# Optimization experiments

Measured on AMD Instinct MI355X. Metric: run time of the kernel, lower is better.

The kernel has to match this reference:

```python
import jax, jax.numpy as jnp
import numpy as np


def setup_inputs() -> dict:
    key = jax.random.key(0)
    ks = jax.random.split(key, 5)
    t, b, s, d = 4, 4, 1024, 512
    x = jax.random.normal(ks[0], (t, b, s, d), dtype=jnp.float32)
    wq = jax.random.normal(ks[1], (d, d), dtype=jnp.float32) * 0.02
    wk = jax.random.normal(ks[2], (d, d), dtype=jnp.float32) * 0.02
    wv = jax.random.normal(ks[3], (d, d), dtype=jnp.float32) * 0.02
    wo = jax.random.normal(ks[4], (d, d), dtype=jnp.float32) * 0.02
    z = jnp.zeros((d,), dtype=jnp.float32)
    return {"x": x, "wq": wq, "bq": z, "wk": wk, "bk": z, "wv": wv,
            "bv": z, "wo": wo, "bo": z, "num_heads": 8}


def reference(x, wq, bq, wk, bk, wv, bv, wo, bo, num_heads):
    t, b, s, d = x.shape
    dh = d // num_heads
    # QKV projections (torch Linear stores weight as [out,in]; here weights are
    # random square matrices so x @ w + b is the same math)
    q = x @ wq + bq
    k = x @ wk + bk
    v = x @ wv + bv
    # Faithful to source: plain row-major view to (t*b*h, s, dh) WITHOUT
    # transposing a head axis (this mixes seq blocks into the batch-of-heads dim)
    q = q.reshape(t * b * num_heads, s, dh)
    k = k.reshape(t * b * num_heads, s, dh)
    v = v.reshape(t * b * num_heads, s, dh)
    scale = 1.0 / jnp.sqrt(jnp.float32(dh))
    scores = jnp.einsum('bqd,bkd->bqk', q, k) * scale  # [t*b*h, s, s]
    attn = jax.nn.softmax(scores, axis=-1)
    out = jnp.einsum('bqk,bkd->bqd', attn, v)  # [t*b*h, s, dh]
    out = out.reshape(t, b, s, d)
    return out @ wo + bo
```

## Files before the change

### kernel.cpp

```cpp
#include <hip/hip_runtime.h>

typedef __bf16 bf16;
typedef __bf16 bf16x4 __attribute__((ext_vector_type(4)));
typedef __bf16 bf16x8 __attribute__((ext_vector_type(8)));
typedef float  f32x4  __attribute__((ext_vector_type(4)));
typedef float  f32x16 __attribute__((ext_vector_type(16)));
typedef unsigned int u32x2 __attribute__((ext_vector_type(2)));
typedef unsigned int u32x4 __attribute__((ext_vector_type(4)));

#define MFMA16(a, b, c) __builtin_amdgcn_mfma_f32_16x16x32_bf16((a), (b), (c), 0, 0, 0)
#define MFMA32(a, b, c) __builtin_amdgcn_mfma_f32_32x32x16_bf16((a), (b), (c), 0, 0, 0)
#define SW(row, g) (((row) << 6) + ((((g) ^ ((row) & 7))) << 3))

#define QSCALE 0.1803368801111137f

typedef __attribute__((address_space(3))) uint32_t       lds_u32_t;
typedef const __attribute__((address_space(1))) uint32_t glob_u32_t;

__device__ __forceinline__ void ld_lds16(const bf16* g, bf16* l) {
    __builtin_amdgcn_global_load_lds((glob_u32_t*)g, (lds_u32_t*)l, 16, 0, 0);
}

template<int OFF>
__device__ __forceinline__ u32x2 tr_b16(uint32_t va) {
    u32x2 d;
    asm volatile("ds_read_b64_tr_b16 %0, %1 offset:%2"
                 : "=v"(d) : "v"(va), "n"(OFF));
    return d;
}

__global__ __launch_bounds__(256) void prep(
    const float* __restrict__ X,
    const float* __restrict__ wq, const float* __restrict__ wk,
    const float* __restrict__ wv, const float* __restrict__ wo,
    bf16* __restrict__ Xb, bf16* __restrict__ wqkvT, bf16* __restrict__ woT)
{
    int bid = blockIdx.x;
    if (bid < 4096) {
        size_t i = ((size_t)bid * 256 + threadIdx.x) * 8;
        const f32x4* s = (const f32x4*)(X + i);
        f32x4 a = s[0], b = s[1];
        bf16x8 o;
        for (int e = 0; e < 4; e++) { o[e] = (bf16)a[e]; o[e + 4] = (bf16)b[e]; }
        *(bf16x8*)(Xb + i) = o;
    } else {
        int idx = (bid - 4096) * 256 + threadIdx.x;
        int which = idx >> 15;
        int r = idx & 32767;
        int kg = r >> 9, n = r & 511;
        const float* w = (which == 0) ? wq : (which == 1) ? wk : (which == 2) ? wv : wo;
        bf16x8 o;
        for (int e = 0; e < 8; e++) o[e] = (bf16)w[(size_t)(kg * 8 + e) * 512 + n];
        bf16* dst = ((which < 3) ? (wqkvT + (size_t)which * 262144) : woT) + (size_t)n * 512 + kg * 8;
        *(bf16x8*)dst = o;
    }
}

__global__ __launch_bounds__(256, 4) void gemm_qkv(
    const bf16* __restrict__ Xb, const bf16* __restrict__ WT,
    const float* __restrict__ bq, const float* __restrict__ bk,
    const float* __restrict__ bv,
    bf16* __restrict__ Q, bf16* __restrict__ K, bf16* __restrict__ V)
{
    __shared__ char smem[34816];
    bf16* As = (bf16*)smem;
    bf16* Bs = (bf16*)(smem + 16384);

    const int t = threadIdx.x;
    const int lane = t & 63, wid = t >> 6;
    const int wr = wid >> 1, wc = wid & 1;
    const int lr = lane & 15, quad = lane >> 4;
    const int bid = blockIdx.x;
    const int xcd = bid & 7, j0 = bid >> 3;
    const int m0 = (xcd * 16 + (j0 & 15)) * 128;
    const int x = j0 >> 4;
    const int which = x >> 2;
    const int n0 = (x & 3) * 128;
    const bf16* Wt = WT + (size_t)which * 262144;

    f32x4 zf = {0.f, 0.f, 0.f, 0.f};
    f32x4 acc[4][4];
    for (int i = 0; i < 4; i++)
        for (int jj = 0; jj < 4; jj++) acc[i][jj] = zf;

    const int srow = t >> 3;
    const int sg = (t & 7) ^ (srow & 7);
    const bf16* gA = Xb + (size_t)(m0 + srow) * 512 + sg * 8;
    const bf16* gB = Wt + (size_t)(n0 + srow) * 512 + sg * 8;
    bf16* lA = As + t * 8;
    bf16* lB = Bs + t * 8;

    for (int k0 = 0; k0 < 512; k0 += 64) {
        for (int p = 0; p < 4; p++) {
            ld_lds16(gA + k0 + p * 32 * 512, lA + p * 2048);
            ld_lds16(gB + k0 + p * 32 * 512, lB + p * 2048);
        }
        __syncthreads();
        for (int kk = 0; kk < 2; ++kk) {
            bf16x8 af[4], bf_[4];
            for (int i = 0; i < 4; i++)
                af[i] = *(const bf16x8*)&As[SW(wr * 64 + i * 16 + lr, kk * 4 + quad)];
            for (int jj = 0; jj < 4; jj++)
                bf_[jj] = *(const bf16x8*)&Bs[SW(wc * 64 + jj * 16 + lr, kk * 4 + quad)];
            for (int i = 0; i < 4; i++)
                for (int jj = 0; jj < 4; jj++)
                    acc[i][jj] = MFMA16(af[i], bf_[jj], acc[i][jj]);
        }
        __syncthreads();
    }

    bf16* OUT = (which == 0) ? Q : (which == 1) ? K : V;
    const float* bias = (which == 0) ? bq : (which == 1) ? bk : bv;
    const float qs = (which == 0) ? QSCALE : 1.0f;

    bf16* Ep = (bf16*)smem + wid * 4352;
    for (int jj = 0; jj < 4; jj++) {
        int n = n0 + wc * 64 + jj * 16 + lr;
        float bb = bias[n];
        for (int i = 0; i < 4; i++) {
            int row = i * 16 + quad * 4;
            for (int r = 0; r < 4; r++)
                Ep[(row + r) * 68 + jj * 16 + lr] = (bf16)((acc[i][jj][r] + bb) * qs);
        }
    }
    bf16* wO = OUT + (size_t)(m0 + wr * 64) * 512 + n0 + wc * 64;
    for (int s = 0; s < 8; s++) {
        int row = s * 8 + (lane >> 3), g = lane & 7;
        *(bf16x8*)(wO + (size_t)row * 512 + g * 8) = *(const bf16x8*)&Ep[row * 68 + g * 8];
    }
}

__global__ __launch_bounds__(256, 4) void gemm_out(
    const bf16* __restrict__ A, const bf16* __restrict__ WoT,
    const float* __restrict__ bo, float* __restrict__ OUT)
{
    __shared__ char smem[34816];
    bf16* As = (bf16*)smem;
    bf16* Bs = (bf16*)(smem + 16384);

    const int t = threadIdx.x;
    const int lane = t & 63, wid = t >> 6;
    const int wr = wid >> 1, wc = wid & 1;
    const int lr = lane & 15, quad = lane >> 4;
    const int bid = blockIdx.x;
    const int xcd = bid & 7, j0 = bid >> 3;
    const int m0 = (xcd * 16 + (j0 & 15)) * 128;
    const int n0 = (j0 >> 4) * 128;

    f32x4 zf = {0.f, 0.f, 0.f, 0.f};
    f32x4 acc[4][4];
    for (int i = 0; i < 4; i++)
        for (int jj = 0; jj < 4; jj++) acc[i][jj] = zf;

    const int srow = t >> 3;
    const int sg = (t & 7) ^ (srow & 7);
    const bf16* gA = A + (size_t)(m0 + srow) * 512 + sg * 8;
    const bf16* gB = WoT + (size_t)(n0 + srow) * 512 + sg * 8;
    bf16* lA = As + t * 8;
    bf16* lB = Bs + t * 8;

    for (int k0 = 0; k0 < 512; k0 += 64) {
        for (int p = 0; p < 4; p++) {
            ld_lds16(gA + k0 + p * 32 * 512, lA + p * 2048);
            ld_lds16(gB + k0 + p * 32 * 512, lB + p * 2048);
        }
        __syncthreads();
        for (int kk = 0; kk < 2; ++kk) {
            bf16x8 af[4], bf_[4];
            for (int i = 0; i < 4; i++)
                af[i] = *(const bf16x8*)&As[SW(wr * 64 + i * 16 + lr, kk * 4 + quad)];
            for (int jj = 0; jj < 4; jj++)
                bf_[jj] = *(const bf16x8*)&Bs[SW(wc * 64 + jj * 16 + lr, kk * 4 + quad)];
            for (int i = 0; i < 4; i++)
                for (int jj = 0; jj < 4; jj++)
                    acc[i][jj] = MFMA16(af[i], bf_[jj], acc[i][jj]);
        }
        __syncthreads();
    }

    float bb[4];
    for (int jj = 0; jj < 4; jj++) bb[jj] = bo[n0 + wc * 64 + jj * 16 + lr];

    float* Ef = (float*)smem + wid * 2112;
    for (int h = 0; h < 2; h++) {
        for (int jj = 0; jj < 4; jj++)
            for (int ii = 0; ii < 2; ii++) {
                int i = h * 2 + ii;
                int row = ii * 16 + quad * 4;
                for (int r = 0; r < 4; r++)
                    Ef[(row + r) * 66 + jj * 16 + lr] = acc[i][jj][r] + bb[jj];
            }
        float* wO = OUT + (size_t)(m0 + wr * 64 + h * 32) * 512 + n0 + wc * 64;
        for (int s = 0; s < 8; s++) {
            int row = s * 4 + (lane >> 4), c = (lane & 15) * 4;
            *(f32x4*)(wO + (size_t)row * 512 + c) = *(const f32x4*)&Ef[row * 66 + c];
        }
        __syncthreads();
    }
}

__global__ __launch_bounds__(256, 4) void attn(
    const bf16* __restrict__ Q, const bf16* __restrict__ K,
    const bf16* __restrict__ V, bf16* __restrict__ O)
{
    __shared__ char smem[32768];
    bf16* const K0 = (bf16*)smem;
    bf16* const V0 = (bf16*)(smem + 8192);
    bf16* const K1 = (bf16*)(smem + 16384);
    bf16* const V1 = (bf16*)(smem + 24576);

    const int t = threadIdx.x, lane = t & 63, wid = t >> 6;
    const int q31 = lane & 31, hi = lane >> 5;
    const int bid = blockIdx.x;
    const int batch = (bid & 7) * 16 + ((bid >> 3) & 15);
    const int q0 = (bid >> 7) * 128;
    const bf16* Qb = Q + (size_t)batch * 65536;
    const bf16* Kb = K + (size_t)batch * 65536;
    const bf16* Vb = V + (size_t)batch * 65536;

    bf16x8 qf[4];
#pragma unroll
    for (int kk = 0; kk < 4; ++kk)
        qf[kk] = *(const bf16x8*)(Qb + (size_t)(q0 + wid * 32 + q31) * 64 + kk * 16 + hi * 8);

    f32x16 oacc[2];
#pragma unroll
    for (int ct = 0; ct < 2; ++ct)
#pragma unroll
        for (int r = 0; r < 16; ++r) oacc[ct][r] = 0.f;
    float lsum = 0.f;

    const int srow = t >> 3;
    const int sg8 = ((t & 7) ^ (srow & 7)) * 8;
    const int vkey = ((t >> 5) << 2) | ((t >> 1) & 3);
    const int vdh  = (((t >> 3) & 3) << 4) | ((t & 1) << 3);

#define STAGE(ktile, KD, VD) do {                                        \
        const bf16* gK_ = Kb + (size_t)(ktile) * 4096;                   \
        const bf16* gV_ = Vb + (size_t)(ktile) * 4096;                   \
        ld_lds16(gK_ + srow * 64 + sg8,          (KD) + t * 8);          \
        ld_lds16(gK_ + (srow + 32) * 64 + sg8,   (KD) + t * 8 + 2048);   \
        ld_lds16(gV_ + vkey * 64 + vdh,          (VD) + t * 8);          \
        ld_lds16(gV_ + (vkey + 32) * 64 + vdh,   (VD) + t * 8 + 2048);   \
    } while (0)

    const uint32_t vaL = ((uint32_t)hi << 10) + (((lane >> 4) & 1) << 7) + ((lane & 15) << 3);
    const uint32_t vaV0 = vaL + 8192u, vaV1 = vaL + 24576u;

    STAGE(0, K0, V0);

    for (int kt = 0; kt < 16; ++kt) {
        bf16* Kt = (kt & 1) ? K1 : K0;
        bf16* Kn = (kt & 1) ? K0 : K1;
        bf16* Vn = (kt & 1) ? V0 : V1;
        const uint32_t va = (kt & 1) ? vaV1 : vaV0;

        __builtin_amdgcn_sched_barrier(0);
        __builtin_amdgcn_s_barrier();
        __builtin_amdgcn_sched_barrier(0);
        if (kt < 15) {
            STAGE(kt + 1, Kn, Vn);
            asm volatile("s_waitcnt vmcnt(4)" ::: "memory");
        } else {
            asm volatile("s_waitcnt vmcnt(0)" ::: "memory");
        }
        __builtin_amdgcn_sched_barrier(0);
        __builtin_amdgcn_s_barrier();
        __builtin_amdgcn_sched_barrier(0);

        f32x16 sacc[2];
#pragma unroll
        for (int i2 = 0; i2 < 2; ++i2)
#pragma unroll
            for (int r = 0; r < 16; ++r) sacc[i2][r] = 0.f;

        __builtin_amdgcn_s_setprio(1);
#pragma unroll
        for (int kk = 0; kk < 4; ++kk) {
            bf16x8 a0 = *(const bf16x8*)&Kt[SW(q31, kk * 2 + hi)];
            bf16x8 a1 = *(const bf16x8*)&Kt[SW(32 + q31, kk * 2 + hi)];
            sacc[0] = MFMA32(a0, qf[kk], sacc[0]);
            sacc[1] = MFMA32(a1, qf[kk], sacc[1]);
        }
        __builtin_amdgcn_s_setprio(0);

        float ls = 0.f;
#pragma unroll
        for (int i2 = 0; i2 < 2; ++i2)
#pragma unroll
            for (int r = 0; r < 16; ++r) {
                float p = __builtin_amdgcn_exp2f(sacc[i2][r]);
                ls += p;
                sacc[i2][r] = p;
            }
        lsum += ls;

        bf16x8 pa[4];
#pragma unroll
        for (int c = 0; c < 4; ++c) {
            const int i2 = c >> 1, rb = (c & 1) * 8;
            uint32_t x0, x1, x2, x3;
            asm("v_cvt_pk_bf16_f32 %0, %1, %2" : "=v"(x0) : "v"(sacc[i2][rb + 0]), "v"(sacc[i2][rb + 1]));
            asm("v_cvt_pk_bf16_f32 %0, %1, %2" : "=v"(x1) : "v"(sacc[i2][rb + 2]), "v"(sacc[i2][rb + 3]));
            asm("v_cvt_pk_bf16_f32 %0, %1, %2" : "=v"(x2) : "v"(sacc[i2][rb + 4]), "v"(sacc[i2][rb + 5]));
            asm("v_cvt_pk_bf16_f32 %0, %1, %2" : "=v"(x3) : "v"(sacc[i2][rb + 6]), "v"(sacc[i2][rb + 7]));
            asm volatile("v_permlane32_swap_b32 %0, %1" : "+v"(x0), "+v"(x2));
            asm volatile("v_permlane32_swap_b32 %0, %1" : "+v"(x1), "+v"(x3));
            u32x4 w = {x0, x1, x2, x3};
            pa[c] = __builtin_bit_cast(bf16x8, w);
        }

        u32x2 tv[4][2][2];
#define TRPAIR(c, ct) do {                                               \
        tv[c][ct][0] = tr_b16<(c) * 2048 + (ct) * 256>(va);              \
        tv[c][ct][1] = tr_b16<(c) * 2048 + (ct) * 256 + 512>(va);        \
    } while (0)
        TRPAIR(0, 0); TRPAIR(0, 1);
        TRPAIR(1, 0); TRPAIR(1, 1);
        TRPAIR(2, 0); TRPAIR(2, 1);
        TRPAIR(3, 0); TRPAIR(3, 1);
#undef TRPAIR

        asm volatile("s_waitcnt lgkmcnt(0)" ::: "memory");
        __builtin_amdgcn_sched_barrier(0);
        __builtin_amdgcn_s_setprio(1);
#pragma unroll
        for (int c = 0; c < 4; ++c)
#pragma unroll
            for (int ct = 0; ct < 2; ++ct) {
                u32x4 w = {tv[c][ct][0][0], tv[c][ct][0][1],
                           tv[c][ct][1][0], tv[c][ct][1][1]};
                oacc[ct] = MFMA32(pa[c], __builtin_bit_cast(bf16x8, w), oacc[ct]);
            }
        __builtin_amdgcn_s_setprio(0);
    }
#undef STAGE

    lsum += __shfl_xor(lsum, 32, 64);
    const float invl = 1.f / lsum;

    __syncthreads();
    bf16* Ep = (bf16*)smem + wid * 2176;
#pragma unroll
    for (int r = 0; r < 16; ++r) {
        const int ql = (r & 3) + 8 * (r >> 2) + 4 * hi;
        const float im = __shfl(invl, ql, 64);
        Ep[ql * 68 + q31]      = (bf16)(oacc[0][r] * im);
        Ep[ql * 68 + 32 + q31] = (bf16)(oacc[1][r] * im);
    }
    bf16* Ob = O + (size_t)batch * 65536 + (size_t)(q0 + wid * 32) * 64;
#pragma unroll
    for (int s = 0; s < 4; s++) {
        int row = s * 8 + (lane >> 3), g = lane & 7;
        *(bf16x8*)(Ob + (size_t)row * 64 + g * 8) = *(const bf16x8*)&Ep[row * 68 + g * 8];
    }
}

extern "C" void kernel_launch(void* const* d_in, const int* in_sizes, int n_in,
                              void* d_out, int out_size, void* d_ws, size_t ws_size,
                              hipStream_t stream)
{
    const float* x  = (const float*)d_in[0];
    const float* wq = (const float*)d_in[1];
    const float* bq = (const float*)d_in[2];
    const float* wk = (const float*)d_in[3];
    const float* bk = (const float*)d_in[4];
    const float* wv = (const float*)d_in[5];
    const float* bv = (const float*)d_in[6];
    const float* wo = (const float*)d_in[7];
    const float* bo = (const float*)d_in[8];

    char* ws = (char*)d_ws;
    bf16* wqkvT = (bf16*)ws;
    bf16* woT   = (bf16*)(ws + 1572864);
    bf16* Xb    = (bf16*)(ws + 2097152);
    bf16* Qb    = (bf16*)(ws + 2097152 + 16777216ull);
    bf16* Kb    = (bf16*)(ws + 2097152 + 2 * 16777216ull);
    bf16* Vb    = (bf16*)(ws + 2097152 + 3 * 16777216ull);
    bf16* Ab    = Xb;

    prep<<<4608, 256, 0, stream>>>(x, wq, wk, wv, wo, Xb, wqkvT, woT);
    gemm_qkv<<<1536, 256, 0, stream>>>(Xb, wqkvT, bq, bk, bv, Qb, Kb, Vb);
    attn<<<1024, 256, 0, stream>>>(Qb, Kb, Vb, Ab);
    gemm_out<<<512, 256, 0, stream>>>(Ab, woT, bo, (float*)d_out);
}
```

Baseline: 189.4 us.

## Double-buffer QKV GEMM LDS tiles with K=32 stages and prefetch

Restructures the QKV projection GEMM main loop. It now uses two LDS buffers with 32-wide K tiles, so the global-to-LDS load for the next K step is issued before the MFMAs on the current buffer. It replaces the single-buffer load, sync, compute, sync loop with explicit barriers, vmcnt waits and a new 32-column swizzle, and raises wave priority around the MFMA block. This is meant to hide global load latency behind compute. In exchange the loop runs twice as many iterations with two barriers each, and the manual waitcnt accounting is fragile.

Result: no change. 191.9 us (+1.4%).

```diff
diff --git a/kernel.cpp b/kernel.cpp
--- a/kernel.cpp
+++ b/kernel.cpp
@@ -11,6 +11,7 @@
 #define MFMA16(a, b, c) __builtin_amdgcn_mfma_f32_16x16x32_bf16((a), (b), (c), 0, 0, 0)
 #define MFMA32(a, b, c) __builtin_amdgcn_mfma_f32_32x32x16_bf16((a), (b), (c), 0, 0, 0)
 #define SW(row, g) (((row) << 6) + ((((g) ^ ((row) & 7))) << 3))
+#define SW32(row, g) (((row) << 5) + ((((g) ^ (((row) >> 1) & 3))) << 3))
 
 #define QSCALE 0.1803368801111137f
 
@@ -63,8 +64,10 @@
     bf16* __restrict__ Q, bf16* __restrict__ K, bf16* __restrict__ V)
 {
     __shared__ char smem[34816];
-    bf16* As = (bf16*)smem;
-    bf16* Bs = (bf16*)(smem + 16384);
+    bf16* const A0 = (bf16*)smem;
+    bf16* const B0 = (bf16*)(smem + 8192);
+    bf16* const A1 = (bf16*)(smem + 16384);
+    bf16* const B1 = (bf16*)(smem + 24576);
 
     const int t = threadIdx.x;
     const int lane = t & 63, wid = t >> 6;
@@ -83,35 +86,63 @@
     for (int i = 0; i < 4; i++)
         for (int jj = 0; jj < 4; jj++) acc[i][jj] = zf;
 
-    const int srow = t >> 3;
-    const int sg = (t & 7) ^ (srow & 7);
+    const int srow = t >> 2;
+    const int sg = (t & 3) ^ ((t >> 3) & 3);
     const bf16* gA = Xb + (size_t)(m0 + srow) * 512 + sg * 8;
     const bf16* gB = Wt + (size_t)(n0 + srow) * 512 + sg * 8;
-    bf16* lA = As + t * 8;
-    bf16* lB = Bs + t * 8;
-
-    for (int k0 = 0; k0 < 512; k0 += 64) {
-        for (int p = 0; p < 4; p++) {
-            ld_lds16(gA + k0 + p * 32 * 512, lA + p * 2048);
-            ld_lds16(gB + k0 + p * 32 * 512, lB + p * 2048);
-        }
-        __syncthreads();
-        for (int kk = 0; kk < 2; ++kk) {
-            bf16x8 af[4], bf_[4];
-            for (int i = 0; i < 4; i++)
-                af[i] = *(const bf16x8*)&As[SW(wr * 64 + i * 16 + lr, kk * 4 + quad)];
+
+#define GSTAGE(kt, AD, BD) do {                                          \
+        const int k0_ = (kt) * 32;                                       \
+        ld_lds16(gA + k0_,            (AD) + t * 8);                     \
+        ld_lds16(gA + k0_ + 64 * 512, (AD) + t * 8 + 2048);              \
+        ld_lds16(gB + k0_,            (BD) + t * 8);                     \
+        ld_lds16(gB + k0_ + 64 * 512, (BD) + t * 8 + 2048);              \
+    } while (0)
+
+    GSTAGE(0, A0, B0);
+
+#pragma unroll
+    for (int kt = 0; kt < 16; ++kt) {
+        const bf16* As = (kt & 1) ? A1 : A0;
+        const bf16* Bs = (kt & 1) ? B1 : B0;
+        bf16* An = (kt & 1) ? A0 : A1;
+        bf16* Bn = (kt & 1) ? B0 : B1;
+
+        __builtin_amdgcn_sched_barrier(0);
+        __builtin_amdgcn_s_barrier();
+        __builtin_amdgcn_sched_barrier(0);
+        if (kt < 15) {
+            GSTAGE(kt + 1, An, Bn);
+            asm volatile("s_waitcnt vmcnt(4)" ::: "memory");
+        } else {
+            asm volatile("s_waitcnt vmcnt(0)" ::: "memory");
+        }
+        __builtin_amdgcn_sched_barrier(0);
+        __builtin_amdgcn_s_barrier();
+        __builtin_amdgcn_sched_barrier(0);
+
+        bf16x8 af[4], bf_[4];
+#pragma unroll
+        for (int i = 0; i < 4; i++)
+            af[i] = *(const bf16x8*)&As[SW32(wr * 64 + i * 16 + lr, quad)];
+#pragma unroll
+        for (int jj = 0; jj < 4; jj++)
+            bf_[jj] = *(const bf16x8*)&Bs[SW32(wc * 64 + jj * 16 + lr, quad)];
+        __builtin_amdgcn_s_setprio(1);
+#pragma unroll
+        for (int i = 0; i < 4; i++)
+#pragma unroll
             for (int jj = 0; jj < 4; jj++)
-                bf_[jj] = *(const bf16x8*)&Bs[SW(wc * 64 + jj * 16 + lr, kk * 4 + quad)];
-            for (int i = 0; i < 4; i++)
-                for (int jj = 0; jj < 4; jj++)
-                    acc[i][jj] = MFMA16(af[i], bf_[jj], acc[i][jj]);
-        }
-        __syncthreads();
-    }
+                acc[i][jj] = MFMA16(af[i], bf_[jj], acc[i][jj]);
+        __builtin_amdgcn_s_setprio(0);
+    }
+#undef GSTAGE
 
     bf16* OUT = (which == 0) ? Q : (which == 1) ? K : V;
     const float* bias = (which == 0) ? bq : (which == 1) ? bk : bv;
     const float qs = (which == 0) ? QSCALE : 1.0f;
+
+    __syncthreads();
 
     bf16* Ep = (bf16*)smem + wid * 4352;
     for (int jj = 0; jj < 4; jj++) {
```
